# Kernel optimization log

Measured on AMD Instinct MI355X. Metric: run time of the kernel, lower is better.

The kernel has to match this reference:

```python
import jax, jax.numpy as jnp
import numpy as np

NEG_INF = -1e30  # safe stand-in for -inf (avoids nan in grads, exp underflows to 0)
STOP_IX, CONT_IX = 0, 1


def setup_inputs() -> dict:
    key = jax.random.key(0)
    k1, k2, k3, k4, k5 = jax.random.split(key, 5)
    B, maxT, b, A = 64, 4096, 16, 18
    action_logps = jax.nn.log_softmax(jax.random.normal(k1, (B, maxT + 1, b, A), jnp.float32), axis=-1)
    stop_logps = jax.nn.log_softmax(jax.random.normal(k2, (B, maxT + 1, b, 2), jnp.float32), axis=-1)
    start_logps = jax.nn.log_softmax(jax.random.normal(k3, (B, maxT + 1, b), jnp.float32), axis=-1)
    actions = jax.random.randint(k4, (B, maxT), 0, A, jnp.int32)
    lengths = jax.random.randint(k5, (B,), maxT // 2, maxT + 1, jnp.int32)
    return {"action_logps": action_logps, "stop_logps": stop_logps,
            "start_logps": start_logps, "actions": actions, "lengths": lengths}


def reference(action_logps, stop_logps, start_logps, actions, lengths):
    """Batched, masked HMM forward algorithm.

    action_logps: (B, maxT+1, b, A); stop_logps: (B, maxT+1, b, 2);
    start_logps: (B, maxT+1, b); actions: (B, maxT) int; lengths: (B,) int.
    Returns scalar: -sum_b logp(traj_b).
    """
    B, Tp1, b, A = action_logps.shape
    maxT = Tp1 - 1
    eye = jnp.eye(b, dtype=bool)  # (b, b)

    # f_0 = start_logps[0] + action_logps[0, :, actions[0]]
    al0 = jnp.take_along_axis(action_logps[:, 0], actions[:, 0][:, None, None], axis=2)[..., 0]  # (B, b)
    f0 = start_logps[:, 0] + al0

    def step(f, i):
        beta = stop_logps[:, i, :, STOP_IX]      # (B, b)
        omb = stop_logps[:, i, :, CONT_IX]       # (B, b)
        cont = jnp.where(eye, omb[:, :, None], NEG_INF)                       # (B, b, b) diag
        trans = jnp.logaddexp(beta[:, :, None] + start_logps[:, i, None, :], cont)  # (B, b, b)
        al = jnp.take_along_axis(action_logps[:, i], actions[:, i][:, None, None], axis=2)[..., 0]  # (B, b)
        f_un = f[:, :, None] + trans + al[:, None, :]                          # (B, b, b)
        f_new = jax.scipy.special.logsumexp(f_un, axis=1)                      # (B, b)
        mask = (i < lengths)[:, None]  # original loop runs i = 1..T-1
        return jnp.where(mask, f_new, f), None

    f, _ = jax.lax.scan(step, f0, jnp.arange(1, maxT))

    # total_logp = logsumexp(f + stop_logps[T, :, STOP]) per trajectory
    stop_all = stop_logps[..., STOP_IX]  # (B, Tp1, b)
    stop_T = jnp.take_along_axis(stop_all, lengths[:, None, None].astype(jnp.int32), axis=1)[:, 0]  # (B, b)
    total_logp = jax.scipy.special.logsumexp(f + stop_T, axis=1)  # (B,)
    return -jnp.sum(total_logp)
```

## Files before the change

### kernel.cpp

```cpp
#include <hip/hip_runtime.h>

#define NEGF (-1e30f)

__device__ __forceinline__ float colmax(float v) {
  v = fmaxf(v, __shfl_xor(v, 1));
  v = fmaxf(v, __shfl_xor(v, 2));
  return v;
}
__device__ __forceinline__ float colsum(float v) {
  v += __shfl_xor(v, 1);
  v += __shfl_xor(v, 2);
  return v;
}

struct Step {
  float beta[4], cont[4], start[4], al[4];
};

__device__ __forceinline__ void load_step(
    const float* __restrict__ actl, const float* __restrict__ stopl,
    const float* __restrict__ startl, long bt , int aidx,
    int A, int r, Step& s)
{
  const float4* sp = reinterpret_cast<const float4*>(stopl + bt * 32 + r * 8);
  float4 s0 = sp[0];
  float4 s1 = sp[1];
  s.beta[0] = s0.x; s.cont[0] = s0.y; s.beta[1] = s0.z; s.cont[1] = s0.w;
  s.beta[2] = s1.x; s.cont[2] = s1.y; s.beta[3] = s1.z; s.cont[3] = s1.w;
  float4 st = *reinterpret_cast<const float4*>(startl + bt * 16 + r * 4);
  s.start[0] = st.x; s.start[1] = st.y; s.start[2] = st.z; s.start[3] = st.w;
  const float* ap = actl + bt * (16L * A) + (long)(r * 4) * A + aidx;
  s.al[0] = ap[0];
  s.al[1] = ap[A];
  s.al[2] = ap[2 * A];
  s.al[3] = ap[3 * A];
}

__global__ __launch_bounds__(256) void hmm_chunks(
    const float* __restrict__ action_logps,
    const float* __restrict__ stop_logps,
    const float* __restrict__ start_logps,
    const int* __restrict__ actions,
    const int* __restrict__ lengths,
    float* __restrict__ Mws, float* __restrict__ Offws,
    int B, int maxT, int A, int NC, int CHUNK)
{
  const int lane = threadIdx.x & 63;
  const int gw = blockIdx.x * (blockDim.x >> 6) + (threadIdx.x >> 6);
  if (gw >= B * NC) return;
  const int batch = gw / NC;
  const int chunk = gw % NC;
  const long Tp1 = (long)maxT + 1;
  const int m = lane >> 2;
  const int r = lane & 3;

  float M[4];
#pragma unroll
  for (int q = 0; q < 4; ++q) M[q] = (4 * r + q == m) ? 0.f : NEGF;
  float off = 0.f;

  const int len = lengths[batch];
  const int i0 = 1 + chunk * CHUNK;
  int i1 = i0 + CHUNK;
  if (i1 > maxT) i1 = maxT;
  if (i1 > len) i1 = len;

  if (i0 < i1) {
    const int* actp = actions + (long)batch * maxT;
    const long bt0 = (long)batch * Tp1;
    Step cur, nxt;
    int aidx1;
    {
      int aidx0 = actp[i0];
      load_step(action_logps, stop_logps, start_logps, bt0 + i0, aidx0, A, r, cur);
      aidx1 = (i0 + 1 < i1) ? actp[i0 + 1] : 0;
    }
    for (int i = i0; i < i1; ++i) {
      const bool more = (i + 1 < i1);
      if (more)
        load_step(action_logps, stop_logps, start_logps, bt0 + i + 1, aidx1, A, r, nxt);
      const int aidx2 = (i + 2 < i1) ? actp[i + 2] : 0;

      float cmax = fmaxf(fmaxf(M[0], M[1]), fmaxf(M[2], M[3]));
      cmax = colmax(cmax);
      float Ms[4];
#pragma unroll
      for (int q = 0; q < 4; ++q) Ms[q] = M[q] - cmax;

      float p = __expf(cur.beta[0] + Ms[0]) + __expf(cur.beta[1] + Ms[1]) +
                __expf(cur.beta[2] + Ms[2]) + __expf(cur.beta[3] + Ms[3]);
      const float ssum = colsum(p);

#pragma unroll
      for (int q = 0; q < 4; ++q) {
        const float e2 = __expf(cur.cont[q] + Ms[q]);
        const float es = __expf(cur.start[q]);
        M[q] = cur.al[q] + __logf(fmaxf(ssum * es + e2, 1e-37f));
      }
      off += cmax;

      cur = nxt;
      aidx1 = aidx2;
    }
  }

  float4 mv = make_float4(M[0], M[1], M[2], M[3]);
  *reinterpret_cast<float4*>(Mws + (long)gw * 256 + (m * 16 + r * 4)) = mv;
  if (r == 0) Offws[(long)gw * 16 + m] = off;
}

__global__ __launch_bounds__(256) void hmm_combine(
    const float* __restrict__ action_logps,
    const float* __restrict__ stop_logps,
    const float* __restrict__ start_logps,
    const int* __restrict__ actions,
    const int* __restrict__ lengths,
    const float* __restrict__ Mws, const float* __restrict__ Offws,
    float* __restrict__ out,
    int B, int maxT, int A, int NC)
{
  const int batch = blockIdx.x * (blockDim.x >> 6) + (threadIdx.x >> 6);
  if (batch >= B) return;
  const int lane = threadIdx.x & 63;
  const int k = lane & 15;
  const int jg = lane >> 4;
  const long Tp1 = (long)maxT + 1;

  const int a0 = actions[(long)batch * maxT];
  float f = start_logps[(long)batch * Tp1 * 16 + k] +
            action_logps[(long)batch * Tp1 * (16L * A) + (long)k * A + a0];

  const float* Mb = Mws + (long)batch * NC * 256;
  const float* Ob = Offws + (long)batch * NC * 16;

  constexpr int PF = 4;
  float pm[PF][4], po[PF][4];
#pragma unroll
  for (int d = 0; d < PF; ++d) {
#pragma unroll
    for (int q = 0; q < 4; ++q) {
      pm[d][q] = Mb[d * 256 + (4 * jg + q) * 16 + k];
      po[d][q] = Ob[d * 16 + 4 * jg + q];
    }
  }

  for (int cb = 0; cb < NC; cb += PF) {
#pragma unroll
    for (int u = 0; u < PF; ++u) {
      const int c = cb + u;
      float v[4];
      float mx = NEGF;
#pragma unroll
      for (int q = 0; q < 4; ++q) {
        const float fj = __shfl(f, 4 * jg + q);
        v[q] = pm[u][q] + po[u][q] + fj;
        mx = fmaxf(mx, v[q]);
      }
      mx = fmaxf(mx, __shfl_xor(mx, 16));
      mx = fmaxf(mx, __shfl_xor(mx, 32));
      float s = 0.f;
#pragma unroll
      for (int q = 0; q < 4; ++q) s += __expf(v[q] - mx);
      s += __shfl_xor(s, 16);
      s += __shfl_xor(s, 32);
      f = mx + __logf(s);

      const int cn = c + PF;
      if (cn < NC) {
#pragma unroll
        for (int q = 0; q < 4; ++q) {
          pm[u][q] = Mb[(long)cn * 256 + (4 * jg + q) * 16 + k];
          po[u][q] = Ob[cn * 16 + 4 * jg + q];
        }
      }
    }
  }

  const int L = lengths[batch];
  const float st = stop_logps[((long)batch * Tp1 + L) * 32 + k * 2];
  const float v = f + st;
  float mx = v;
  mx = fmaxf(mx, __shfl_xor(mx, 1));
  mx = fmaxf(mx, __shfl_xor(mx, 2));
  mx = fmaxf(mx, __shfl_xor(mx, 4));
  mx = fmaxf(mx, __shfl_xor(mx, 8));
  float s = __expf(v - mx);
  s += __shfl_xor(s, 1);
  s += __shfl_xor(s, 2);
  s += __shfl_xor(s, 4);
  s += __shfl_xor(s, 8);
  const float tot = mx + __logf(s);
  if (lane == 0) atomicAdd(out, -tot);
}

extern "C" void kernel_launch(void* const* d_in, const int* in_sizes, int n_in,
                              void* d_out, int out_size, void* d_ws, size_t ws_size,
                              hipStream_t stream) {
  const float* action_logps = (const float*)d_in[0];
  const float* stop_logps = (const float*)d_in[1];
  const float* start_logps = (const float*)d_in[2];
  const int* actions = (const int*)d_in[3];
  const int* lengths = (const int*)d_in[4];

  const int B = in_sizes[4];
  const int maxT = in_sizes[3] / B;
  const long Tp1 = (long)maxT + 1;
  const int b = (int)((long)in_sizes[1] / ((long)B * Tp1 * 2));
  const int A = (int)((long)in_sizes[0] / ((long)B * Tp1 * b));
  (void)b;

  int NC = 64;
  const size_t per_chunk = (size_t)B * (256 + 16) * sizeof(float);
  if ((size_t)NC * per_chunk > ws_size) {
    NC = (int)(ws_size / per_chunk) & ~3;
    if (NC < 4) NC = 4;
  }
  const int CHUNK = (maxT - 1 + NC - 1) / NC;

  float* Mws = (float*)d_ws;
  float* Offws = Mws + (size_t)B * NC * 256;

  hipMemsetAsync(d_out, 0, (size_t)out_size * sizeof(float), stream);

  const int nwaves = B * NC;
  hmm_chunks<<<dim3((nwaves + 3) / 4), dim3(256), 0, stream>>>(
      action_logps, stop_logps, start_logps, actions, lengths,
      Mws, Offws, B, maxT, A, NC, CHUNK);
  hmm_combine<<<dim3((B + 3) / 4), dim3(256), 0, stream>>>(
      action_logps, stop_logps, start_logps, actions, lengths,
      Mws, Offws, (float*)d_out, B, maxT, A, NC);
}
```

Measured before the change: 468.1 us.

## Deepen step prefetch to two ahead, precompute exp(start), double chunk count

The chunk kernel now prefetches step data two iterations ahead instead of one, and loads action indices four steps ahead. It computes exp(start) at load time, so the exponential sits off the serial dependency chain. The number of chunks per batch goes from 64 to 128, which doubles the parallel waves and halves the serial chain length per wave. The cost is more registers per wave and a longer sequential combine pass over the extra chunks.

```diff
diff --git a/kernel.cpp b/kernel.cpp
--- a/kernel.cpp
+++ b/kernel.cpp
@@ -14,7 +14,7 @@
 }
 
 struct Step {
-  float beta[4], cont[4], start[4], al[4];
+  float beta[4], cont[4], es[4], al[4];
 };
 
 __device__ __forceinline__ void load_step(
@@ -28,7 +28,8 @@
   s.beta[0] = s0.x; s.cont[0] = s0.y; s.beta[1] = s0.z; s.cont[1] = s0.w;
   s.beta[2] = s1.x; s.cont[2] = s1.y; s.beta[3] = s1.z; s.cont[3] = s1.w;
   float4 st = *reinterpret_cast<const float4*>(startl + bt * 16 + r * 4);
-  s.start[0] = st.x; s.start[1] = st.y; s.start[2] = st.z; s.start[3] = st.w;
+  s.es[0] = __expf(st.x); s.es[1] = __expf(st.y);
+  s.es[2] = __expf(st.z); s.es[3] = __expf(st.w);
   const float* ap = actl + bt * (16L * A) + (long)(r * 4) * A + aidx;
   s.al[0] = ap[0];
   s.al[1] = ap[A];
@@ -68,18 +69,19 @@
   if (i0 < i1) {
     const int* actp = actions + (long)batch * maxT;
     const long bt0 = (long)batch * Tp1;
-    Step cur, nxt;
-    int aidx1;
-    {
-      int aidx0 = actp[i0];
-      load_step(action_logps, stop_logps, start_logps, bt0 + i0, aidx0, A, r, cur);
-      aidx1 = (i0 + 1 < i1) ? actp[i0 + 1] : 0;
-    }
+    const int n = i1 - i0;
+    Step cur, n1, n2;
+    load_step(action_logps, stop_logps, start_logps, bt0 + i0, actp[i0], A, r, cur);
+    if (n > 1)
+      load_step(action_logps, stop_logps, start_logps, bt0 + i0 + 1, actp[i0 + 1], A, r, n1);
+    int a2 = (n > 2) ? actp[i0 + 2] : 0;
+    int a3 = (n > 3) ? actp[i0 + 3] : 0;
+
     for (int i = i0; i < i1; ++i) {
-      const bool more = (i + 1 < i1);
-      if (more)
-        load_step(action_logps, stop_logps, start_logps, bt0 + i + 1, aidx1, A, r, nxt);
-      const int aidx2 = (i + 2 < i1) ? actp[i + 2] : 0;
+      if (i + 2 < i1)
+        load_step(action_logps, stop_logps, start_logps, bt0 + i + 2, a2, A, r, n2);
+      a2 = a3;
+      a3 = (i + 4 < i1) ? actp[i + 4] : 0;
 
       float cmax = fmaxf(fmaxf(M[0], M[1]), fmaxf(M[2], M[3]));
       cmax = colmax(cmax);
@@ -94,13 +96,12 @@
 #pragma unroll
       for (int q = 0; q < 4; ++q) {
         const float e2 = __expf(cur.cont[q] + Ms[q]);
-        const float es = __expf(cur.start[q]);
-        M[q] = cur.al[q] + __logf(fmaxf(ssum * es + e2, 1e-37f));
+        M[q] = cur.al[q] + __logf(fmaxf(ssum * cur.es[q] + e2, 1e-37f));
       }
       off += cmax;
 
-      cur = nxt;
-      aidx1 = aidx2;
+      cur = n1;
+      n1 = n2;
     }
   }
 
@@ -209,7 +210,7 @@
   const int A = (int)((long)in_sizes[0] / ((long)B * Tp1 * b));
   (void)b;
 
-  int NC = 64;
+  int NC = 128;
   const size_t per_chunk = (size_t)B * (256 + 16) * sizeof(float);
   if ((size_t)NC * per_chunk > ws_size) {
     NC = (int)(ws_size / per_chunk) & ~3;
```

Result: slower. 502.6 us (+7.4%).
